# Kernel tuning notes

Hardware: AMD Instinct MI355X
Metric: run time of the kernel (lower is better)

Reference implementation:

```python
import jax, jax.numpy as jnp
import numpy as np

N_HASHES = 4
CHUNK = 144
REDUCTION = 4
RES_SCALE = 0.1
L2_EPS = 5e-5


def _conv(x, w, b):
    # keras Conv2D, strides 1, padding 'same', NHWC/HWIO
    return jax.lax.conv_general_dilated(
        x, w, window_strides=(1, 1), padding='SAME',
        dimension_numbers=('NHWC', 'HWIO', 'NHWC')) + b


def setup_inputs() -> dict:
    key = jax.random.key(0)
    ks = jax.random.split(key, 4)
    N, H, W, Ch = 4, 96, 96, 256
    C = Ch // REDUCTION
    hb = min((H * W) // CHUNK + ((H * W) // CHUNK) % 2, 128)  # = 64
    return {
        'input': jax.random.normal(ks[0], (N, H, W, Ch), jnp.float32),
        'w_match': jax.random.normal(ks[1], (3, 3, Ch, C), jnp.float32) * 0.02,
        'b_match': jnp.zeros((C,), jnp.float32),
        'w_asm': jax.random.normal(ks[2], (3, 3, Ch, Ch), jnp.float32) * 0.02,
        'b_asm': jnp.zeros((Ch,), jnp.float32),
        'rotations': jax.random.normal(ks[3], (C, N_HASHES, hb // 2), jnp.float32),
    }


def reference(input, w_match, b_match, w_asm, b_asm, rotations):
    N, H, W, Ch = input.shape
    L = H * W
    C = Ch // REDUCTION
    nh = N_HASHES

    xm = _conv(input, w_match, b_match)   # (N,H,W,C)
    ya = _conv(input, w_asm, b_asm)       # (N,H,W,Ch)
    # Faithful to the TF code: reshape NHWC buffer to (N, C, L) then transpose.
    x_embed = xm.reshape(N, -1, L).transpose(0, 2, 1)  # (N, L, C)
    y_embed = ya.reshape(N, -1, L).transpose(0, 2, 1)  # (N, L, Ch)

    hash_buckets = min(L // CHUNK + (L // CHUNK) % 2, 128)
    # LSH: random rotations shared across batch
    rot = jnp.einsum('btf,fhi->bhti', x_embed, rotations)       # (N,nh,L,hb/2)
    rot = jnp.concatenate([rot, -rot], axis=-1)                 # (N,nh,L,hb)
    codes = jnp.argmax(rot, axis=-1).astype(jnp.int32)          # (N,nh,L)
    codes = codes + (jnp.arange(nh, dtype=jnp.int32) * hash_buckets)[None, :, None]
    codes = codes.reshape(N, -1)                                # (N, nh*L)

    idx = jnp.argsort(codes, axis=-1)
    undo_sort = jnp.argsort(idx, axis=-1)
    mod = idx % L

    xs = jnp.take_along_axis(x_embed, mod[..., None], axis=1)   # (N, nh*L, C)
    ys = jnp.take_along_axis(y_embed, mod[..., None], axis=1)   # (N, nh*L, Ch)

    pad = (CHUNK - L % CHUNK) % CHUNK
    xb = xs.reshape(N, nh, L, C)
    yb = ys.reshape(N, nh, L, Ch)
    if pad:
        xb = jnp.concatenate([xb, xb[:, :, -pad:]], axis=2)
        yb = jnp.concatenate([yb, yb[:, :, -pad:]], axis=2)
    xb = xb.reshape(N, nh, -1, CHUNK, C)    # (N,nh,K,chunk,C)
    yb = yb.reshape(N, nh, -1, CHUNK, Ch)

    # tf.math.l2_normalize: x * rsqrt(max(sum(x^2), eps))
    ss = jnp.sum(xb * xb, axis=-1, keepdims=True)
    x_match = xb * jax.lax.rsqrt(jnp.maximum(ss, L2_EPS))

    def add_adjacent(t):  # concat bucket, bucket-1, bucket+1 along chunk axis
        return jnp.concatenate(
            [t, jnp.roll(t, 1, axis=2), jnp.roll(t, -1, axis=2)], axis=3)

    x_match = add_adjacent(x_match)         # (N,nh,K,3*chunk,C)
    y3 = add_adjacent(yb)                   # (N,nh,K,3*chunk,Ch)

    raw = jnp.einsum('bhkie,bhkje->bhkij', xb, x_match)  # (N,nh,K,chunk,3chunk)
    lse = jax.scipy.special.logsumexp(raw, axis=-1, keepdims=True)
    score = jnp.exp(raw - lse)
    ret = jnp.einsum('bhkij,bhkje->bhkie', score, y3)    # (N,nh,K,chunk,Ch)

    ret = ret.reshape(N, nh, -1, Ch)
    bs = lse.reshape(N, nh, -1)
    if pad:
        ret = ret[:, :, :-pad]
        bs = bs[:, :, :-pad]

    ret = ret.reshape(N, nh * L, Ch)
    bs = bs.reshape(N, nh * L)
    ret = jnp.take_along_axis(ret, undo_sort[..., None], axis=1)
    bs = jnp.take_along_axis(bs, undo_sort, axis=1)

    ret = ret.reshape(N, nh, L, Ch)
    probs = jax.nn.softmax(bs.reshape(N, nh, L, 1), axis=1)
    ret = jnp.sum(ret * probs, axis=1)      # (N, L, Ch)

    ret = ret.transpose(0, 2, 1).reshape(N, H, W, Ch)  # inverse of the TF reshape
    return ret * RES_SCALE + input
```

## Files before the change

kernel.cpp:

```cpp
#include <hip/hip_runtime.h>
#include <cstdint>
#include <cstddef>

#define NB 4
#define HH 96
#define WW 96
#define CHN 256
#define CC 64
#define LL 9216
#define NHASH 4
#define HBK 64
#define CHK 144
#define NCHUNK 64
#define NJ 36864

typedef __attribute__((ext_vector_type(8))) short bf16x8;
typedef __attribute__((ext_vector_type(8))) unsigned short u16x8;
typedef __attribute__((ext_vector_type(4))) float f32x4;

__device__ __forceinline__ unsigned short f2b(float f) {
    unsigned int x = __float_as_uint(f);
    x += 0x7FFFu + ((x >> 16) & 1u);
    return (unsigned short)(x >> 16);
}
__device__ __forceinline__ float b2f(unsigned short u) {
    return __uint_as_float(((unsigned int)u) << 16);
}

__global__ __launch_bounds__(256) void cvt_in_hilo_k(const float* __restrict__ in,
                                                     unsigned short* __restrict__ hi,
                                                     unsigned short* __restrict__ lo)
{
    size_t g = ((size_t)blockIdx.x * 256 + threadIdx.x) * 8;
    float4 v0 = *(const float4*)(in + g);
    float4 v1 = *(const float4*)(in + g + 4);
    float xs[8] = {v0.x, v0.y, v0.z, v0.w, v1.x, v1.y, v1.z, v1.w};
    u16x8 h, l;
#pragma unroll
    for (int i = 0; i < 8; i++) {
        unsigned short hv = f2b(xs[i]);
        h[i] = hv;
        l[i] = f2b(xs[i] - b2f(hv));
    }
    *(u16x8*)(hi + g) = h;
    *(u16x8*)(lo + g) = l;
}

__global__ __launch_bounds__(256) void cvt_wm_hilo_k(const float* __restrict__ w,
                                                     unsigned short* __restrict__ hiT,
                                                     unsigned short* __restrict__ loT)
{
    __shared__ float tl[32][33];
    const int tap = blockIdx.z;
    const int c0 = blockIdx.x * 32;
    const int o0 = blockIdx.y * 32;
    const int tx = threadIdx.x & 31, ty0 = threadIdx.x >> 5;
#pragma unroll
    for (int i = 0; i < 32; i += 8)
        tl[ty0 + i][tx] = w[((size_t)tap * 256 + c0 + ty0 + i) * 64 + o0 + tx];
    __syncthreads();
#pragma unroll
    for (int i = 0; i < 32; i += 8) {
        float v = tl[tx][ty0 + i];
        unsigned short h = f2b(v);
        size_t o = ((size_t)tap * 64 + o0 + ty0 + i) * 256 + c0 + tx;
        hiT[o] = h;
        loT[o] = f2b(v - b2f(h));
    }
}

#define ASTR 40
__global__ __launch_bounds__(256, 2) void conv_match_mfma_k(
    const unsigned short* __restrict__ in_hi, const unsigned short* __restrict__ in_lo,
    const unsigned short* __restrict__ wmT_hi, const unsigned short* __restrict__ wmT_lo,
    const float* __restrict__ bias, float* __restrict__ xm)
{
    __shared__ short Ah[64 * ASTR], Al[64 * ASTR];
    __shared__ short Bh[64 * ASTR], Bl[64 * ASTR];
    const int n = blockIdx.z, p0 = blockIdx.x * 64;
    const int tid = threadIdx.x;
    const int w = tid >> 6;
    const int lane = tid & 63, lm = lane & 15, lq = lane >> 4;
    const int r = tid >> 2, q8 = (tid & 3) * 8;
    const int p = p0 + r, py = p / WW, px = p % WW;
    const unsigned short* hiN = in_hi + (size_t)n * LL * CHN;
    const unsigned short* loN = in_lo + (size_t)n * LL * CHN;

    f32x4 acc[4];
#pragma unroll
    for (int b = 0; b < 4; b++) acc[b] = (f32x4){0.f, 0.f, 0.f, 0.f};

    for (int tap = 0; tap < 9; tap++) {
        const int ky = tap / 3, kx = tap - ky * 3;
        const int sy = py + ky - 1, sx = px + kx - 1;
        const bool valid = ((unsigned)sy < HH) && ((unsigned)sx < WW);
        const unsigned short* ah = hiN + (size_t)(sy * WW + sx) * CHN + q8;
        const unsigned short* al = loN + (size_t)(sy * WW + sx) * CHN + q8;
        const unsigned short* bh = wmT_hi + ((size_t)tap * 64 + r) * 256 + q8;
        const unsigned short* bl = wmT_lo + ((size_t)tap * 64 + r) * 256 + q8;
        for (int ci0 = 0; ci0 < 256; ci0 += 32) {
            u16x8 avh = (u16x8){0,0,0,0,0,0,0,0}, avl = (u16x8){0,0,0,0,0,0,0,0};
            if (valid) {
                avh = *(const u16x8*)(ah + ci0);
                avl = *(const u16x8*)(al + ci0);
            }
            u16x8 bvh = *(const u16x8*)(bh + ci0);
            u16x8 bvl = *(const u16x8*)(bl + ci0);
            __syncthreads();
            *(u16x8*)&Ah[r * ASTR + q8] = avh;
            *(u16x8*)&Al[r * ASTR + q8] = avl;
            *(u16x8*)&Bh[r * ASTR + q8] = bvh;
            *(u16x8*)&Bl[r * ASTR + q8] = bvl;
            __syncthreads();
            bf16x8 afh = *(const bf16x8*)&Ah[(w * 16 + lm) * ASTR + lq * 8];
            bf16x8 afl = *(const bf16x8*)&Al[(w * 16 + lm) * ASTR + lq * 8];
#pragma unroll
            for (int nt = 0; nt < 4; nt++) {
                bf16x8 bfh = *(const bf16x8*)&Bh[(nt * 16 + lm) * ASTR + lq * 8];
                bf16x8 bfl = *(const bf16x8*)&Bl[(nt * 16 + lm) * ASTR + lq * 8];
                acc[nt] = __builtin_amdgcn_mfma_f32_16x16x32_bf16(afh, bfh, acc[nt], 0, 0, 0);
                acc[nt] = __builtin_amdgcn_mfma_f32_16x16x32_bf16(afh, bfl, acc[nt], 0, 0, 0);
                acc[nt] = __builtin_amdgcn_mfma_f32_16x16x32_bf16(afl, bfh, acc[nt], 0, 0, 0);
            }
        }
    }
    float bvv[4];
#pragma unroll
    for (int nt = 0; nt < 4; nt++) bvv[nt] = bias[nt * 16 + lm];
    float* outN = xm + (size_t)n * LL * 64;
#pragma unroll
    for (int r4 = 0; r4 < 4; r4++) {
        int row = p0 + w * 16 + lq * 4 + r4;
        float* od = outN + (size_t)row * 64;
#pragma unroll
        for (int nt = 0; nt < 4; nt++)
            od[nt * 16 + lm] = acc[nt][r4] + bvv[nt];
    }
}

__global__ __launch_bounds__(256) void transpose_k(const float* __restrict__ in, float* __restrict__ out,
                                                   unsigned short* __restrict__ out_bf, int R, int Cc)
{
    __shared__ float tl[32][33];
    const int n = blockIdx.z;
    const size_t base = (size_t)n * R * Cc;
    int c0 = blockIdx.x * 32, r0 = blockIdx.y * 32;
    int tx = threadIdx.x & 31, ty0 = threadIdx.x >> 5;
#pragma unroll
    for (int i = 0; i < 32; i += 8)
        tl[ty0 + i][tx] = in[base + (size_t)(r0 + ty0 + i) * Cc + c0 + tx];
    __syncthreads();
#pragma unroll
    for (int i = 0; i < 32; i += 8) {
        float v = tl[tx][ty0 + i];
        size_t o = base + (size_t)(c0 + ty0 + i) * R + r0 + tx;
        out[o] = v;
        out_bf[o] = f2b(v);
    }
}

__global__ __launch_bounds__(256) void cvt_wT_k(const float* __restrict__ w, unsigned short* __restrict__ wT)
{
    __shared__ float tl[32][33];
    const int tap = blockIdx.z;
    const int c0 = blockIdx.x * 32;
    const int o0 = blockIdx.y * 32;
    const int tx = threadIdx.x & 31, ty0 = threadIdx.x >> 5;
#pragma unroll
    for (int i = 0; i < 32; i += 8)
        tl[ty0 + i][tx] = w[((size_t)tap * 256 + c0 + ty0 + i) * 256 + o0 + tx];
    __syncthreads();
#pragma unroll
    for (int i = 0; i < 32; i += 8)
        wT[((size_t)tap * 256 + o0 + ty0 + i) * 256 + c0 + tx] = f2b(tl[tx][ty0 + i]);
}

__global__ __launch_bounds__(256) void conv_mfma_k(
    const unsigned short* __restrict__ in_bf, const unsigned short* __restrict__ wT,
    const float* __restrict__ bias, unsigned short* __restrict__ ya_bf)
{
    __shared__ short As[128 * 32];
    __shared__ short Bs[128 * 32];
    const int n = blockIdx.z, p0 = blockIdx.x * 128, co0 = blockIdx.y * 128;
    const int tid = threadIdx.x;
    const int w = tid >> 6, wr = w >> 1, wc = w & 1;
    const int lane = tid & 63, lm = lane & 15, lq = lane >> 4;
    const int r = tid >> 1, hf = tid & 1;
    const int p = p0 + r, py = p / WW, px = p % WW;
    const unsigned short* inN = in_bf + (size_t)n * LL * CHN;

    f32x4 acc[4][4];
#pragma unroll
    for (int a = 0; a < 4; a++)
#pragma unroll
        for (int b = 0; b < 4; b++) acc[a][b] = (f32x4){0.f, 0.f, 0.f, 0.f};

    for (int tap = 0; tap < 9; tap++) {
        const int ky = tap / 3, kx = tap - ky * 3;
        const int sy = py + ky - 1, sx = px + kx - 1;
        const bool valid = ((unsigned)sy < HH) && ((unsigned)sx < WW);
        const unsigned short* asrc = inN + (size_t)(sy * WW + sx) * CHN + hf * 16;
        const unsigned short* bsrc = wT + ((size_t)tap * 256 + co0 + r) * 256 + hf * 16;
        for (int ci0 = 0; ci0 < 256; ci0 += 32) {
            u16x8 av0 = (u16x8){0,0,0,0,0,0,0,0}, av1 = (u16x8){0,0,0,0,0,0,0,0};
            if (valid) {
                av0 = *(const u16x8*)(asrc + ci0);
                av1 = *(const u16x8*)(asrc + ci0 + 8);
            }
            u16x8 bv0 = *(const u16x8*)(bsrc + ci0);
            u16x8 bv1 = *(const u16x8*)(bsrc + ci0 + 8);
            __syncthreads();
            *(u16x8*)&As[r * 32 + hf * 16]     = av0;
            *(u16x8*)&As[r * 32 + hf * 16 + 8] = av1;
            *(u16x8*)&Bs[r * 32 + hf * 16]     = bv0;
            *(u16x8*)&Bs[r * 32 + hf * 16 + 8] = bv1;
            __syncthreads();
            bf16x8 af[4], bf[4];
#pragma unroll
            for (int mt = 0; mt < 4; mt++)
                af[mt] = *(const bf16x8*)&As[(wr * 64 + mt * 16 + lm) * 32 + lq * 8];
#pragma unroll
            for (int nt = 0; nt < 4; nt++)
                bf[nt] = *(const bf16x8*)&Bs[(wc * 64 + nt * 16 + lm) * 32 + lq * 8];
#pragma unroll
            for (int mt = 0; mt < 4; mt++)
#pragma unroll
                for (int nt = 0; nt < 4; nt++)
                    acc[mt][nt] = __builtin_amdgcn_mfma_f32_16x16x32_bf16(af[mt], bf[nt], acc[mt][nt], 0, 0, 0);
        }
    }
    float bv[4];
#pragma unroll
    for (int nt = 0; nt < 4; nt++) bv[nt] = bias[co0 + wc * 64 + nt * 16 + lm];
#pragma unroll
    for (int mt = 0; mt < 4; mt++) {
#pragma unroll
        for (int r4 = 0; r4 < 4; r4++) {
            int row = p0 + wr * 64 + mt * 16 + lq * 4 + r4;
            unsigned short* od = ya_bf + ((size_t)n * LL + row) * CHN + co0 + wc * 64;
#pragma unroll
            for (int nt = 0; nt < 4; nt++)
                od[nt * 16 + lm] = f2b(acc[mt][nt][r4] + bv[nt]);
        }
    }
}

__global__ __launch_bounds__(256) void transpose_bf_k(const unsigned short* __restrict__ in,
                                                      unsigned short* __restrict__ out)
{
    __shared__ unsigned short tl[64][65];
    const int n = blockIdx.z;
    const size_t base = (size_t)n * LL * CHN;
    const int t0 = blockIdx.x * 64, e0 = blockIdx.y * 64;
    const int tx = threadIdx.x & 63, ty0 = threadIdx.x >> 6;
#pragma unroll
    for (int i = 0; i < 16; i++) {
        int row = ty0 + i * 4;
        tl[row][tx] = in[base + (size_t)(e0 + row) * LL + t0 + tx];
    }
    __syncthreads();
#pragma unroll
    for (int i = 0; i < 16; i++) {
        int row = ty0 + i * 4;
        out[base + (size_t)(t0 + row) * CHN + e0 + tx] = tl[tx][row];
    }
}

__global__ __launch_bounds__(256) void hash_k(const float* __restrict__ xmT, const float* __restrict__ rot,
                                              int* __restrict__ codes, float* __restrict__ ssq)
{
    __shared__ float rs[32 * 68];
    const int h = blockIdx.y;
    for (int e = threadIdx.x; e < 2048; e += 256) {
        int hi = e >> 6, f = e & 63;
        rs[hi * 68 + f] = rot[f * 128 + h * 32 + hi];
    }
    __syncthreads();
    int g = blockIdx.x * 256 + threadIdx.x;
    int n = g / LL, t = g % LL;
    float4 x4[16];
    const float* src = xmT + (size_t)g * CC;
#pragma unroll
    for (int f4 = 0; f4 < 16; f4++) x4[f4] = *(const float4*)(src + f4 * 4);
    if (h == 0) {
        float ss = 0.f;
#pragma unroll
        for (int f4 = 0; f4 < 16; f4++)
            ss += x4[f4].x * x4[f4].x + x4[f4].y * x4[f4].y + x4[f4].z * x4[f4].z + x4[f4].w * x4[f4].w;
        ssq[g] = ss;
    }
    float bp = -1e30f, bn = -1e30f;
    int ip = 0, inn = 0;
    for (int i = 0; i < 32; i++) {
        const float* rr = &rs[i * 68];
        float d0 = 0.f, d1 = 0.f, d2 = 0.f, d3 = 0.f;
#pragma unroll
        for (int f4 = 0; f4 < 16; f4++) {
            float4 r4 = *(const float4*)(rr + f4 * 4);
            d0 = fmaf(x4[f4].x, r4.x, d0);
            d1 = fmaf(x4[f4].y, r4.y, d1);
            d2 = fmaf(x4[f4].z, r4.z, d2);
            d3 = fmaf(x4[f4].w, r4.w, d3);
        }
        float d = (d0 + d1) + (d2 + d3);
        if (d > bp) { bp = d; ip = i; }
        if (-d > bn) { bn = -d; inn = i; }
    }
    int code = (bp >= bn) ? ip : (32 + inn);
    codes[(size_t)n * NJ + h * LL + t] = code + h * HBK;
}

__global__ __launch_bounds__(256) void sort_hist_k(const int* __restrict__ codes, int* __restrict__ hist,
                                                   int* __restrict__ rank)
{
    __shared__ int lhw[4][256];
    const int n = blockIdx.y, seg = blockIdx.x, tid = threadIdx.x;
    const int w = tid >> 6, lane = tid & 63;
    int j = seg * 256 + tid;
    int c = codes[(size_t)n * NJ + j];
    for (int e = tid; e < 1024; e += 256) ((int*)lhw)[e] = 0;
    __syncthreads();
    unsigned long long eq = ~0ull;
#pragma unroll
    for (int b = 0; b < 8; b++) {
        unsigned long long m = __ballot((c >> b) & 1);
        eq &= ((c >> b) & 1) ? m : ~m;
    }
    int rw = __popcll(eq & ((1ull << lane) - 1ull));
    int cntw = __popcll(eq);
    if (rw == 0) lhw[w][c] = cntw;
    __syncthreads();
    int base = 0;
    if (w > 0) base += lhw[0][c];
    if (w > 1) base += lhw[1][c];
    if (w > 2) base += lhw[2][c];
    rank[(size_t)n * NJ + j] = base + rw;
    hist[(size_t)n * NJ + tid * 144 + seg] = lhw[0][tid] + lhw[1][tid] + lhw[2][tid] + lhw[3][tid];
}

__global__ __launch_bounds__(256) void sort_scan_k(int* __restrict__ hist)
{
    const int n = blockIdx.x;
    const int key = threadIdx.x;
    int* hn = hist + (size_t)n * NJ;
    int sum = 0;
    for (int s = 0; s < 144; s++) sum += hn[key * 144 + s];
    __shared__ int sc[256];
    sc[key] = sum;
    __syncthreads();
    for (int off = 1; off < 256; off <<= 1) {
        int v = (key >= off) ? sc[key - off] : 0;
        __syncthreads();
        sc[key] += v;
        __syncthreads();
    }
    int run = sc[key] - sum;
    for (int s = 0; s < 144; s++) { int v = hn[key * 144 + s]; hn[key * 144 + s] = run; run += v; }
}

__global__ __launch_bounds__(256) void sort_scatter_k(const int* __restrict__ codes, const int* __restrict__ rank,
                                                      const int* __restrict__ hist, int* __restrict__ sidx,
                                                      int* __restrict__ undo)
{
    const int n = blockIdx.y, seg = blockIdx.x, tid = threadIdx.x;
    int j = seg * 256 + tid;
    int c = codes[(size_t)n * NJ + j];
    int dest = hist[(size_t)n * NJ + c * 144 + seg] + rank[(size_t)n * NJ + j];
    sidx[(size_t)n * NJ + dest] = j;
    undo[(size_t)n * NJ + j] = dest;
}

#define QSTR 72
#define PSTR 164
__global__ __launch_bounds__(1024, 4) __attribute__((amdgpu_waves_per_eu(4, 4))) void attn_mfma_k(
    const unsigned short* __restrict__ xmT_bf, const unsigned short* __restrict__ yaT,
    const float* __restrict__ ssq, const int* __restrict__ sidx,
    unsigned short* __restrict__ Osort, float* __restrict__ bs)
{
    __shared__ short Qs[144 * QSTR];
    __shared__ short Ks[144 * QSTR];
    __shared__ short Ps[144 * PSTR];
    __shared__ int   tIdx[432];
    __shared__ int   voff[432];
    __shared__ float nfs[432];
    __shared__ float qlen[432];
    __shared__ float lsum[144];
    __shared__ float linv[144];

    const int k = blockIdx.x, h = blockIdx.y, n = blockIdx.z;
    const int tid = threadIdx.x;
    const int w = tid >> 6, lane = tid & 63;
    const int lm = lane & 15, lq = lane >> 4;
    const size_t sbase = (size_t)n * NJ + (size_t)h * LL;

    if (tid < 432) {
        int cc = tid / CHK, rr = tid - cc * CHK;
        int c = (cc == 0) ? k : (cc == 1 ? (k + NCHUNK - 1) & (NCHUNK - 1) : (k + 1) & (NCHUNK - 1));
        int j = sidx[sbase + c * CHK + rr];
        int t = j % LL;
        tIdx[tid] = t;
        voff[tid] = t * (CHN * 2);
        float m = fmaxf(ssq[(size_t)n * LL + t], 5e-5f);
        float nf = rsqrtf(m);
        nfs[tid] = nf;
        qlen[tid] = m * nf;
    }
    __syncthreads();

    const int sr = tid >> 3, sj = (tid & 7) * 8;
    const int sr2 = (tid + 1024) >> 3, sj2 = (tid & 7) * 8;
    {
        u16x8 v = *(const u16x8*)(xmT_bf + ((size_t)n * LL + tIdx[sr]) * CC + sj);
        *(u16x8*)&Qs[sr * QSTR + sj] = v;
        if (tid < 128) {
            u16x8 v2 = *(const u16x8*)(xmT_bf + ((size_t)n * LL + tIdx[sr2]) * CC + sj2);
            *(u16x8*)&Qs[sr2 * QSTR + sj2] = v2;
        }
    }
    for (int e = tid; e < 2304; e += 1024) {
        int r = e >> 4, c = 144 + (e & 15);
        Ps[r * PSTR + c] = 0;
    }
    u16x8 kreg0, kreg1;
    kreg0 = *(const u16x8*)(xmT_bf + ((size_t)n * LL + tIdx[CHK + sr]) * CC + sj);
    if (tid < 128)
        kreg1 = *(const u16x8*)(xmT_bf + ((size_t)n * LL + tIdx[CHK + sr2]) * CC + sj2);

    const char* vbase = (const char*)(yaT + (size_t)n * LL * CHN + w * 16 + lm);
    f32x4 accO[9];
#pragma unroll
    for (int mt = 0; mt < 9; mt++) accO[mt] = (f32x4){0.f, 0.f, 0.f, 0.f};
    f32x4 accL = (f32x4){0.f, 0.f, 0.f, 0.f};
    bf16x8 onesF, onesL;
#pragma unroll
    for (int i = 0; i < 8; i++) {
        onesF[i] = (short)0x3F80;
        onesL[i] = (lq < 2) ? (short)0x3F80 : (short)0;
    }

    for (int cc = 0; cc < 3; cc++) {
        const int c144 = cc * CHK;
        if (cc > 0) {
            *(u16x8*)&Ks[sr * QSTR + sj] = kreg0;
            if (tid < 128) *(u16x8*)&Ks[sr2 * QSTR + sj2] = kreg1;
        }
        if (cc < 2) {
            kreg0 = *(const u16x8*)(xmT_bf + ((size_t)n * LL + tIdx[(cc + 1) * CHK + sr]) * CC + sj);
            if (tid < 128)
                kreg1 = *(const u16x8*)(xmT_bf + ((size_t)n * LL + tIdx[(cc + 1) * CHK + sr2]) * CC + sj2);
        }
        bf16x8 vfrag[5];
#pragma unroll
        for (int ks = 0; ks < 5; ks++) {
            int kb = ks * 32 + lq * 8;
            if (kb < 144) {
                int4 o0 = *(const int4*)&voff[c144 + kb];
                int4 o1 = *(const int4*)&voff[c144 + kb + 4];
                vfrag[ks][0] = (short)*(const unsigned short*)(vbase + o0.x);
                vfrag[ks][1] = (short)*(const unsigned short*)(vbase + o0.y);
                vfrag[ks][2] = (short)*(const unsigned short*)(vbase + o0.z);
                vfrag[ks][3] = (short)*(const unsigned short*)(vbase + o0.w);
                vfrag[ks][4] = (short)*(const unsigned short*)(vbase + o1.x);
                vfrag[ks][5] = (short)*(const unsigned short*)(vbase + o1.y);
                vfrag[ks][6] = (short)*(const unsigned short*)(vbase + o1.z);
                vfrag[ks][7] = (short)*(const unsigned short*)(vbase + o1.w);
            } else {
                vfrag[ks] = (bf16x8){0, 0, 0, 0, 0, 0, 0, 0};
            }
        }
        __syncthreads();

        const short* Bsrc = (cc == 0) ? Qs : Ks;
        for (int tt = w; tt < 81; tt += 16) {
            int mt = tt / 9, nt = tt - mt * 9;
            f32x4 c = {0.f, 0.f, 0.f, 0.f};
#pragma unroll
            for (int ks = 0; ks < 2; ks++) {
                bf16x8 a = *(const bf16x8*)&Qs[(mt * 16 + lm) * QSTR + ks * 32 + lq * 8];
                bf16x8 b = *(const bf16x8*)&Bsrc[(nt * 16 + lm) * QSTR + ks * 32 + lq * 8];
                c = __builtin_amdgcn_mfma_f32_16x16x32_bf16(a, b, c, 0, 0, 0);
            }
            float nfk = nfs[c144 + nt * 16 + lm];
#pragma unroll
            for (int r = 0; r < 4; r++) {
                int mrow = mt * 16 + lq * 4 + r;
                float p = __expf(fmaf(c[r], nfk, -qlen[mrow]));
                Ps[mrow * PSTR + nt * 16 + lm] = (short)f2b(p);
            }
        }
        __syncthreads();

        if (w < 9) {
#pragma unroll
            for (int ks = 0; ks < 5; ks++) {
                bf16x8 a = *(const bf16x8*)&Ps[(w * 16 + lm) * PSTR + ks * 32 + lq * 8];
                accL = __builtin_amdgcn_mfma_f32_16x16x32_bf16(a, (ks == 4) ? onesL : onesF, accL, 0, 0, 0);
            }
        }
#pragma unroll
        for (int mt = 0; mt < 9; mt++) {
            f32x4 c = accO[mt];
#pragma unroll
            for (int ks = 0; ks < 5; ks++) {
                bf16x8 a = *(const bf16x8*)&Ps[(mt * 16 + lm) * PSTR + ks * 32 + lq * 8];
                c = __builtin_amdgcn_mfma_f32_16x16x32_bf16(a, vfrag[ks], c, 0, 0, 0);
            }
            accO[mt] = c;
        }
    }

    if (w < 9 && lm == 0) {
#pragma unroll
        for (int r = 0; r < 4; r++) lsum[w * 16 + lq * 4 + r] = accL[r];
    }
    __syncthreads();
    if (tid < 144) {
        float l = lsum[tid];
        linv[tid] = 1.0f / l;
        bs[sbase + tIdx[tid]] = qlen[tid] + __logf(l);
    }
    __syncthreads();

#pragma unroll
    for (int mt = 0; mt < 9; mt++) {
        f32x4 c = accO[mt];
#pragma unroll
        for (int r = 0; r < 4; r++) {
            int mrow = mt * 16 + lq * 4 + r;
            Osort[(sbase + (size_t)k * CHK + mrow) * CHN + w * 16 + lm] = f2b(c[r] * linv[mrow]);
        }
    }
}

__global__ __launch_bounds__(256) void combfin_k(
    const unsigned short* __restrict__ Osort, const float* __restrict__ bs,
    const int* __restrict__ undo, const float* __restrict__ inp, float* __restrict__ out)
{
    __shared__ float ac[32][260];
    __shared__ int   uS[4][32];
    __shared__ float pS[4][32];
    const int n = blockIdx.y;
    const int t0 = blockIdx.x * 32;
    const int tid = threadIdx.x;
    if (tid < 128) {
        int hh = tid >> 5, tt = tid & 31;
        size_t idx = (size_t)n * NJ + (size_t)hh * LL + t0 + tt;
        uS[hh][tt] = undo[idx];
        pS[hh][tt] = bs[idx];
    }
    __syncthreads();
    if (tid < 32) {
        float b0 = pS[0][tid], b1 = pS[1][tid], b2 = pS[2][tid], b3 = pS[3][tid];
        float mx = fmaxf(fmaxf(b0, b1), fmaxf(b2, b3));
        float e0 = __expf(b0 - mx), e1 = __expf(b1 - mx), e2 = __expf(b2 - mx), e3 = __expf(b3 - mx);
        float inv = 1.f / (e0 + e1 + e2 + e3);
        pS[0][tid] = e0 * inv; pS[1][tid] = e1 * inv; pS[2][tid] = e2 * inv; pS[3][tid] = e3 * inv;
    }
    __syncthreads();
    const int g = tid & 63, tq = tid >> 6;
    for (int tt8 = 0; tt8 < 8; tt8++) {
        int t = tq * 8 + tt8;
        float a0 = 0.f, a1 = 0.f, a2 = 0.f, a3 = 0.f;
#pragma unroll
        for (int hh = 0; hh < 4; hh++) {
            int row = uS[hh][t];
            float p = pS[hh][t];
            ushort4 u = *(const ushort4*)&Osort[((size_t)n * NJ + row) * CHN + g * 4];
            a0 = fmaf(p, b2f(u.x), a0);
            a1 = fmaf(p, b2f(u.y), a1);
            a2 = fmaf(p, b2f(u.z), a2);
            a3 = fmaf(p, b2f(u.w), a3);
        }
        *(float4*)&ac[t][g * 4] = make_float4(a0, a1, a2, a3);
    }
    __syncthreads();
    const int tp = tid & 31, er = tid >> 5;
    const float* inN = inp + (size_t)n * LL * CHN;
    float* outN = out + (size_t)n * LL * CHN;
    for (int it = 0; it < 32; it++) {
        int e = er + it * 8;
        size_t o = (size_t)e * LL + t0 + tp;
        outN[o] = ac[tp][e] * 0.1f + inN[o];
    }
}

extern "C" void kernel_launch(void* const* d_in, const int* in_sizes, int n_in,
                              void* d_out, int out_size, void* d_ws, size_t ws_size,
                              hipStream_t stream)
{
    (void)in_sizes; (void)n_in; (void)out_size; (void)ws_size;
    const float* input   = (const float*)d_in[0];
    const float* w_match = (const float*)d_in[1];
    const float* b_match = (const float*)d_in[2];
    const float* w_asm   = (const float*)d_in[3];
    const float* b_asm   = (const float*)d_in[4];
    const float* rot     = (const float*)d_in[5];
    float* out = (float*)d_out;

    char* ws = (char*)d_ws;
    size_t off = 0;
    auto alloc = [&](size_t bytes) -> void* {
        void* p = ws + off;
        off += (bytes + 255) & ~(size_t)255;
        return p;
    };
    unsigned short* in_bf  = (unsigned short*)alloc((size_t)NB * LL * CHN * 2);
    unsigned short* wT_bf  = (unsigned short*)alloc((size_t)9 * CHN * CHN * 2);
    unsigned short* ya_bf  = (unsigned short*)alloc((size_t)NB * LL * CHN * 2);
    unsigned short* yaT    = (unsigned short*)alloc((size_t)NB * LL * CHN * 2);
    float* xm     = (float*)alloc((size_t)NB * LL * CC * 4);
    float* xmT    = (float*)alloc((size_t)NB * LL * CC * 4);
    unsigned short* xmT_bf = (unsigned short*)alloc((size_t)NB * LL * CC * 2);
    float* ssq    = (float*)alloc((size_t)NB * LL * 4);
    int*   codes  = (int*)  alloc((size_t)NB * NJ * 4);
    int*   rank   = (int*)  alloc((size_t)NB * NJ * 4);
    int*   hist   = (int*)  alloc((size_t)NB * NJ * 4);
    int*   sidx   = (int*)  alloc((size_t)NB * NJ * 4);
    int*   undo   = (int*)  alloc((size_t)NB * NJ * 4);
    float* bs     = (float*)alloc((size_t)NB * NJ * 4);
    unsigned short* Osort = (unsigned short*)alloc((size_t)NB * NJ * CHN * 2);
    unsigned short* wmT_hi = (unsigned short*)alloc((size_t)9 * 64 * CHN * 2);
    unsigned short* wmT_lo = (unsigned short*)alloc((size_t)9 * 64 * CHN * 2);
    unsigned short* in_lo = Osort;

    cvt_in_hilo_k<<<dim3(4608), 256, 0, stream>>>(input, in_bf, in_lo);
    cvt_wm_hilo_k<<<dim3(8, 2, 9), 256, 0, stream>>>(w_match, wmT_hi, wmT_lo);
    conv_match_mfma_k<<<dim3(144, 1, NB), 256, 0, stream>>>(in_bf, in_lo, wmT_hi, wmT_lo, b_match, xm);
    transpose_k<<<dim3(288, 2, NB), 256, 0, stream>>>(xm, xmT, xmT_bf, CC, LL);
    cvt_wT_k<<<dim3(8, 8, 9), 256, 0, stream>>>(w_asm, wT_bf);
    conv_mfma_k<<<dim3(72, 2, NB), 256, 0, stream>>>(in_bf, wT_bf, b_asm, ya_bf);
    transpose_bf_k<<<dim3(144, 4, NB), 256, 0, stream>>>(ya_bf, yaT);
    hash_k<<<dim3(144, NHASH), 256, 0, stream>>>(xmT, rot, codes, ssq);
    sort_hist_k<<<dim3(144, NB), 256, 0, stream>>>(codes, hist, rank);
    sort_scan_k<<<dim3(NB), 256, 0, stream>>>(hist);
    sort_scatter_k<<<dim3(144, NB), 256, 0, stream>>>(codes, rank, hist, sidx, undo);
    attn_mfma_k<<<dim3(NCHUNK, NHASH, NB), 1024, 0, stream>>>(xmT_bf, yaT, ssq, sidx, Osort, bs);
    combfin_k<<<dim3(288, NB), 256, 0, stream>>>(Osort, bs, undo, input, out);
}
```

Baseline: 472.8 us.

## Split attention P tile into two row halves to shrink LDS and raise occupancy

The score/probability tile in shared memory is cut from 144 rows to 80, and each chunk is processed in two passes (rows 0-79, then 80-143) that reuse the same P buffer. The launch bound changes from 4 to 8 waves per EU and the explicit waves_per_eu attribute is removed, so more blocks can be resident per CU. In exchange each chunk iteration gains two extra block-wide barriers and a second QK pass, and register pressure under the tighter occupancy target may cause spills.

```diff
diff --git a/kernel.cpp b/kernel.cpp
--- a/kernel.cpp
+++ b/kernel.cpp
@@ -372,14 +372,15 @@
 
 #define QSTR 72
 #define PSTR 164
-__global__ __launch_bounds__(1024, 4) __attribute__((amdgpu_waves_per_eu(4, 4))) void attn_mfma_k(
+#define PROWS 80
+__global__ __launch_bounds__(1024, 8) void attn_mfma_k(
     const unsigned short* __restrict__ xmT_bf, const unsigned short* __restrict__ yaT,
     const float* __restrict__ ssq, const int* __restrict__ sidx,
     unsigned short* __restrict__ Osort, float* __restrict__ bs)
 {
     __shared__ short Qs[144 * QSTR];
     __shared__ short Ks[144 * QSTR];
-    __shared__ short Ps[144 * PSTR];
+    __shared__ short Ps[PROWS * PSTR];
     __shared__ int   tIdx[432];
     __shared__ int   voff[432];
     __shared__ float nfs[432];
@@ -417,7 +418,7 @@
             *(u16x8*)&Qs[sr2 * QSTR + sj2] = v2;
         }
     }
-    for (int e = tid; e < 2304; e += 1024) {
+    for (int e = tid; e < 1280; e += 1024) {
         int r = e >> 4, c = 144 + (e & 15);
         Ps[r * PSTR + c] = 0;
     }
@@ -471,7 +472,7 @@
         __syncthreads();
 
         const short* Bsrc = (cc == 0) ? Qs : Ks;
-        for (int tt = w; tt < 81; tt += 16) {
+        for (int tt = w; tt < 45; tt += 16) {
             int mt = tt / 9, nt = tt - mt * 9;
             f32x4 c = {0.f, 0.f, 0.f, 0.f};
 #pragma unroll
@@ -490,7 +491,7 @@
         }
         __syncthreads();
 
-        if (w < 9) {
+        if (w < 5) {
 #pragma unroll
             for (int ks = 0; ks < 5; ks++) {
                 bf16x8 a = *(const bf16x8*)&Ps[(w * 16 + lm) * PSTR + ks * 32 + lq * 8];
@@ -498,7 +499,7 @@
             }
         }
 #pragma unroll
-        for (int mt = 0; mt < 9; mt++) {
+        for (int mt = 0; mt < 5; mt++) {
             f32x4 c = accO[mt];
 #pragma unroll
             for (int ks = 0; ks < 5; ks++) {
@@ -506,6 +507,45 @@
                 c = __builtin_amdgcn_mfma_f32_16x16x32_bf16(a, vfrag[ks], c, 0, 0, 0);
             }
             accO[mt] = c;
+        }
+        __syncthreads();
+
+        for (int tt = w; tt < 36; tt += 16) {
+            int mt2 = tt / 9, nt = tt - mt2 * 9;
+            int qrow0 = (mt2 + 5) * 16;
+            f32x4 c = {0.f, 0.f, 0.f, 0.f};
+#pragma unroll
+            for (int ks = 0; ks < 2; ks++) {
+                bf16x8 a = *(const bf16x8*)&Qs[(qrow0 + lm) * QSTR + ks * 32 + lq * 8];
+                bf16x8 b = *(const bf16x8*)&Bsrc[(nt * 16 + lm) * QSTR + ks * 32 + lq * 8];
+                c = __builtin_amdgcn_mfma_f32_16x16x32_bf16(a, b, c, 0, 0, 0);
+            }
+            float nfk = nfs[c144 + nt * 16 + lm];
+#pragma unroll
+            for (int r = 0; r < 4; r++) {
+                int mrow = qrow0 + lq * 4 + r;
+                float p = __expf(fmaf(c[r], nfk, -qlen[mrow]));
+                Ps[(mt2 * 16 + lq * 4 + r) * PSTR + nt * 16 + lm] = (short)f2b(p);
+            }
+        }
+        __syncthreads();
+
+        if (w >= 5 && w < 9) {
+#pragma unroll
+            for (int ks = 0; ks < 5; ks++) {
+                bf16x8 a = *(const bf16x8*)&Ps[((w - 5) * 16 + lm) * PSTR + ks * 32 + lq * 8];
+                accL = __builtin_amdgcn_mfma_f32_16x16x32_bf16(a, (ks == 4) ? onesL : onesF, accL, 0, 0, 0);
+            }
+        }
+#pragma unroll
+        for (int mt2 = 0; mt2 < 4; mt2++) {
+            f32x4 c = accO[mt2 + 5];
+#pragma unroll
+            for (int ks = 0; ks < 5; ks++) {
+                bf16x8 a = *(const bf16x8*)&Ps[(mt2 * 16 + lm) * PSTR + ks * 32 + lq * 8];
+                c = __builtin_amdgcn_mfma_f32_16x16x32_bf16(a, vfrag[ks], c, 0, 0, 0);
+            }
+            accO[mt2 + 5] = c;
         }
     }
 
```

New measurement: 570.6 us. +20.7%, slower.
